# Performance work log

Hardware: AMD Instinct MI355X
Metric: run time of the kernel (lower is better)

## Reference

```python
import jax, jax.numpy as jnp
import numpy as np


def setup_inputs() -> dict:
    key = jax.random.key(0)
    k1, k2 = jax.random.split(key)
    B, P, D = 32, 512, 384
    x = jax.random.normal(k1, (B, P, D), dtype=jnp.float32)
    duration = jax.random.randint(k2, (B, P), 0, 5, dtype=jnp.int32)
    return {"x": x, "duration": duration, "max_len": 2048}


def reference(x, duration, max_len):
    # x: [B, P, D], duration: [B, P] int, max_len: python int
    B, P, D = x.shape
    dur = duration.astype(jnp.int32)
    ends = jnp.cumsum(dur, axis=1)          # [B, P] exclusive end offsets per phoneme
    mel_lens = ends[:, -1]                   # [B] total frames per utterance
    t = jnp.arange(max_len, dtype=jnp.int32)
    # frame t belongs to phoneme i where ends[i-1] <= t < ends[i]
    idx = jax.vmap(lambda e: jnp.searchsorted(e, t, side='right'))(ends)  # [B, T]
    idx = jnp.clip(idx, 0, P - 1)
    out = jnp.take_along_axis(x, idx[..., None], axis=1)  # [B, T, D]
    mask = (t[None, :] < mel_lens[:, None])[..., None]     # zero out padding frames
    out = jnp.where(mask, out, jnp.zeros((), dtype=x.dtype))
    return out, mel_lens
```

## Files before the change

### kernel.cpp

```cpp
#include <hip/hip_runtime.h>

#define LR_B      32
#define LR_P      512
#define LR_D      384
#define LR_MAXLEN 2048
#define LR_V4     (LR_D / 4)

__global__ __launch_bounds__(LR_P) void lr_scan_idx(
    const int* __restrict__ dur,
    int* __restrict__ idx_out,
    float* __restrict__ mel_out)
{
    const int b   = blockIdx.x;
    const int tid = threadIdx.x;

    __shared__ int s[LR_P];
    s[tid] = dur[b * LR_P + tid];
    __syncthreads();

    #pragma unroll
    for (int off = 1; off < LR_P; off <<= 1) {
        int v = (tid >= off) ? s[tid - off] : 0;
        __syncthreads();
        s[tid] += v;
        __syncthreads();
    }

    const int mel = s[LR_P - 1];
    if (tid == 0) mel_out[b] = (float)mel;

    #pragma unroll
    for (int k = 0; k < LR_MAXLEN / LR_P; ++k) {
        const int t = tid + k * LR_P;
        int r;
        if (t >= mel) {
            r = -1;
        } else {
            int lo = 0, hi = LR_P;
            while (lo < hi) {
                int mid = (lo + hi) >> 1;
                if (s[mid] <= t) lo = mid + 1; else hi = mid;
            }
            r = lo;
        }
        idx_out[b * LR_MAXLEN + t] = r;
    }
}

__global__ __launch_bounds__(256) void lr_gather(
    const float4* __restrict__ x4,
    const int*    __restrict__ idx,
    float4*       __restrict__ out4)
{
    const int gid   = blockIdx.x * 256 + threadIdx.x;
    const int frame = gid / LR_V4;
    const int v     = gid - frame * LR_V4;

    const int p = idx[frame];
    float4 val;
    if (p >= 0) {
        const int b = frame >> 11;
        val = x4[(b * LR_P + p) * LR_V4 + v];
    } else {
        val = make_float4(0.f, 0.f, 0.f, 0.f);
    }
    out4[gid] = val;
}

extern "C" void kernel_launch(void* const* d_in, const int* in_sizes, int n_in,
                              void* d_out, int out_size, void* d_ws, size_t ws_size,
                              hipStream_t stream)
{
    const float* x   = (const float*)d_in[0];
    const int*   dur = (const int*)d_in[1];

    float* out = (float*)d_out;
    float* mel = out + (size_t)LR_B * LR_MAXLEN * LR_D;

    int* ws_idx = (int*)d_ws;

    lr_scan_idx<<<LR_B, LR_P, 0, stream>>>(dur, ws_idx, mel);

    const int total4 = LR_B * LR_MAXLEN * LR_V4;
    lr_gather<<<total4 / 256, 256, 0, stream>>>(
        (const float4*)x, ws_idx, (float4*)out);
}
```

Measured before the change: 28.78 us.

## Use wave-shuffle scan, two float4s per thread, XCD remap and nontemporal stores

The block-wide shared-memory scan is replaced with a wavefront shuffle scan plus a small cross-wave prefix, which cuts the number of barriers. The gather kernel now has each thread move two float4 halves of a frame, so it launches half as many blocks. Block IDs are remapped so that each of the 8 XCDs handles a contiguous chunk. Outputs are written with nontemporal stores to avoid polluting the cache. These changes target memory-bound write bandwidth and scan latency, and they reduce the number of threads available to hide memory latency.

```diff
diff --git a/kernel.cpp b/kernel.cpp
--- a/kernel.cpp
+++ b/kernel.cpp
@@ -5,28 +5,42 @@
 #define LR_D      384
 #define LR_MAXLEN 2048
 #define LR_V4     (LR_D / 4)
+#define LR_HV4    (LR_V4 / 2)
+
+typedef float f32x4 __attribute__((ext_vector_type(4)));
 
 __global__ __launch_bounds__(LR_P) void lr_scan_idx(
     const int* __restrict__ dur,
     int* __restrict__ idx_out,
     float* __restrict__ mel_out)
 {
-    const int b   = blockIdx.x;
-    const int tid = threadIdx.x;
+    const int b    = blockIdx.x;
+    const int tid  = threadIdx.x;
+    const int lane = tid & 63;
+    const int wid  = tid >> 6;
 
-    __shared__ int s[LR_P];
-    s[tid] = dur[b * LR_P + tid];
+    __shared__ int ends[LR_P];
+    __shared__ int wsum[LR_P / 64];
+
+    int v = dur[b * LR_P + tid];
+
+    #pragma unroll
+    for (int off = 1; off < 64; off <<= 1) {
+        int u = __shfl_up(v, off, 64);
+        if (lane >= off) v += u;
+    }
+    if (lane == 63) wsum[wid] = v;
     __syncthreads();
 
+    int woff = 0;
     #pragma unroll
-    for (int off = 1; off < LR_P; off <<= 1) {
-        int v = (tid >= off) ? s[tid - off] : 0;
-        __syncthreads();
-        s[tid] += v;
-        __syncthreads();
-    }
+    for (int i = 0; i < LR_P / 64; ++i)
+        woff += (i < wid) ? wsum[i] : 0;
+    v += woff;
+    ends[tid] = v;
+    __syncthreads();
 
-    const int mel = s[LR_P - 1];
+    const int mel = ends[LR_P - 1];
     if (tid == 0) mel_out[b] = (float)mel;
 
     #pragma unroll
@@ -39,7 +53,7 @@
             int lo = 0, hi = LR_P;
             while (lo < hi) {
                 int mid = (lo + hi) >> 1;
-                if (s[mid] <= t) lo = mid + 1; else hi = mid;
+                if (ends[mid] <= t) lo = mid + 1; else hi = mid;
             }
             r = lo;
         }
@@ -47,24 +61,36 @@
     }
 }
 
+#define LR_GBLOCKS ((LR_B * LR_MAXLEN * LR_HV4) / 256)
+#define LR_NXCD    8
+#define LR_CHUNK   (LR_GBLOCKS / LR_NXCD)
+
 __global__ __launch_bounds__(256) void lr_gather(
-    const float4* __restrict__ x4,
-    const int*    __restrict__ idx,
-    float4*       __restrict__ out4)
+    const f32x4* __restrict__ x4,
+    const int*   __restrict__ idx,
+    f32x4*       __restrict__ out4)
 {
-    const int gid   = blockIdx.x * 256 + threadIdx.x;
-    const int frame = gid / LR_V4;
-    const int v     = gid - frame * LR_V4;
+    const int bid = blockIdx.x;
+    const int lb  = (bid & (LR_NXCD - 1)) * LR_CHUNK + (bid >> 3);
+
+    const int gid   = lb * 256 + threadIdx.x;
+    const int frame = gid / LR_HV4;
+    const int v0    = gid - frame * LR_HV4;
 
     const int p = idx[frame];
-    float4 val;
+    f32x4 a, c;
     if (p >= 0) {
-        const int b = frame >> 11;
-        val = x4[(b * LR_P + p) * LR_V4 + v];
+        const int b    = frame >> 11;
+        const int base = (b * LR_P + p) * LR_V4 + v0;
+        a = x4[base];
+        c = x4[base + LR_HV4];
     } else {
-        val = make_float4(0.f, 0.f, 0.f, 0.f);
+        a = (f32x4){0.f, 0.f, 0.f, 0.f};
+        c = a;
     }
-    out4[gid] = val;
+    const int obase = frame * LR_V4 + v0;
+    __builtin_nontemporal_store(a, &out4[obase]);
+    __builtin_nontemporal_store(c, &out4[obase + LR_HV4]);
 }
 
 extern "C" void kernel_launch(void* const* d_in, const int* in_sizes, int n_in,
@@ -81,7 +107,6 @@
 
     lr_scan_idx<<<LR_B, LR_P, 0, stream>>>(dur, ws_idx, mel);
 
-    const int total4 = LR_B * LR_MAXLEN * LR_V4;
-    lr_gather<<<total4 / 256, 256, 0, stream>>>(
-        (const float4*)x, ws_idx, (float4*)out);
+    lr_gather<<<LR_GBLOCKS, 256, 0, stream>>>(
+        (const f32x4*)x, ws_idx, (f32x4*)out);
 }
```

Result: faster. 26.74 us (-7.1%).

## Fuse duration scan and frame gather into one kernel with per-block recomputed scan

Applied to the files above, without the earlier changes.

Replaces the two-kernel pipeline (block scan plus binary search writing an index buffer, then a gather) with a single kernel. Each block recomputes the wavefront-shuffle prefix sum over its utterance's durations and scatters phoneme indices for its 32-frame chunk into shared memory, so the workspace round trip and one launch disappear. Blocks are remapped across XCDs so that chunks of the same utterance land on the same XCD, and output stores use nontemporal hints. In exchange, the duration scan is recomputed redundantly in every block.

```diff
diff --git a/kernel.cpp b/kernel.cpp
--- a/kernel.cpp
+++ b/kernel.cpp
@@ -5,66 +5,88 @@
 #define LR_D      384
 #define LR_MAXLEN 2048
 #define LR_V4     (LR_D / 4)
+#define LR_FPB    32
+#define LR_F4PB   (LR_FPB * LR_V4)
+#define LR_THREADS 256
+#define LR_F4PT   (LR_F4PB / LR_THREADS)
 
-__global__ __launch_bounds__(LR_P) void lr_scan_idx(
-    const int* __restrict__ dur,
-    int* __restrict__ idx_out,
-    float* __restrict__ mel_out)
+#define LR_CHUNKS  (LR_MAXLEN / LR_FPB)
+#define LR_GBLOCKS (LR_B * LR_CHUNKS)
+#define LR_NXCD    8
+#define LR_CPX     (LR_GBLOCKS / LR_NXCD)
+
+typedef float f32x4 __attribute__((ext_vector_type(4)));
+
+__global__ __launch_bounds__(LR_THREADS) void lr_fused(
+    const int*   __restrict__ dur,
+    const f32x4* __restrict__ x4,
+    f32x4*       __restrict__ out4,
+    float*       __restrict__ mel_out)
 {
-    const int b   = blockIdx.x;
-    const int tid = threadIdx.x;
+    const int bid = blockIdx.x;
+    const int lb  = (bid & (LR_NXCD - 1)) * LR_CPX + (bid >> 3);
 
-    __shared__ int s[LR_P];
-    s[tid] = dur[b * LR_P + tid];
+    const int b    = lb >> 6;
+    const int c    = lb & 63;
+    const int base = c * LR_FPB;
+
+    const int tid  = threadIdx.x;
+    const int lane = tid & 63;
+    const int wid  = tid >> 6;
+
+    __shared__ int smem_idx[LR_FPB];
+    __shared__ int wsum[LR_THREADS / 64];
+
+    if (tid < LR_FPB) smem_idx[tid] = -1;
+
+    const int2 d2 = ((const int2*)(dur + b * LR_P))[tid];
+    const int  e0 = d2.x, e1 = d2.y;
+    int s = e0 + e1;
+
+    #pragma unroll
+    for (int off = 1; off < 64; off <<= 1) {
+        int u = __shfl_up(s, off, 64);
+        if (lane >= off) s += u;
+    }
+    if (lane == 63) wsum[wid] = s;
     __syncthreads();
 
+    int woff = 0, total = 0;
     #pragma unroll
-    for (int off = 1; off < LR_P; off <<= 1) {
-        int v = (tid >= off) ? s[tid - off] : 0;
-        __syncthreads();
-        s[tid] += v;
-        __syncthreads();
+    for (int i = 0; i < LR_THREADS / 64; ++i) {
+        int w = wsum[i];
+        woff  += (i < wid) ? w : 0;
+        total += w;
     }
+    const int ends1  = s + woff;
+    const int ends0  = ends1 - e1;
+    const int start0 = ends0 - e0;
 
-    const int mel = s[LR_P - 1];
-    if (tid == 0) mel_out[b] = (float)mel;
+    {
+        int lo = max(start0, base), hi = min(ends0, base + LR_FPB);
+        for (int f = lo; f < hi; ++f) smem_idx[f - base] = 2 * tid;
+        lo = max(ends0, base);  hi = min(ends1, base + LR_FPB);
+        for (int f = lo; f < hi; ++f) smem_idx[f - base] = 2 * tid + 1;
+    }
+    if (c == 0 && tid == 0) mel_out[b] = (float)total;
+    __syncthreads();
 
+    const f32x4* xb    = x4 + (size_t)b * LR_P * LR_V4;
+    f32x4*       ob    = out4 + ((size_t)b * LR_MAXLEN + base) * LR_V4;
     #pragma unroll
-    for (int k = 0; k < LR_MAXLEN / LR_P; ++k) {
-        const int t = tid + k * LR_P;
-        int r;
-        if (t >= mel) {
-            r = -1;
+    for (int k = 0; k < LR_F4PT; ++k) {
+        const unsigned j     = tid + k * LR_THREADS;
+        const unsigned frame = j / LR_V4;
+        const unsigned v     = j - frame * LR_V4;
+        const int p = smem_idx[frame];
+        f32x4 val;
+        if (p >= 0) {
+            val = xb[(unsigned)p * LR_V4 + v];
         } else {
-            int lo = 0, hi = LR_P;
-            while (lo < hi) {
-                int mid = (lo + hi) >> 1;
-                if (s[mid] <= t) lo = mid + 1; else hi = mid;
-            }
-            r = lo;
+            val = (f32x4){0.f, 0.f, 0.f, 0.f};
         }
-        idx_out[b * LR_MAXLEN + t] = r;
+        __builtin_nontemporal_store(val, &ob[j]);
     }
-}
-
-__global__ __launch_bounds__(256) void lr_gather(
-    const float4* __restrict__ x4,
-    const int*    __restrict__ idx,
-    float4*       __restrict__ out4)
-{
-    const int gid   = blockIdx.x * 256 + threadIdx.x;
-    const int frame = gid / LR_V4;
-    const int v     = gid - frame * LR_V4;
-
-    const int p = idx[frame];
-    float4 val;
-    if (p >= 0) {
-        const int b = frame >> 11;
-        val = x4[(b * LR_P + p) * LR_V4 + v];
-    } else {
-        val = make_float4(0.f, 0.f, 0.f, 0.f);
-    }
-    out4[gid] = val;
 }
 
 extern "C" void kernel_launch(void* const* d_in, const int* in_sizes, int n_in,
@@ -77,11 +99,6 @@
     float* out = (float*)d_out;
     float* mel = out + (size_t)LR_B * LR_MAXLEN * LR_D;
 
-    int* ws_idx = (int*)d_ws;
-
-    lr_scan_idx<<<LR_B, LR_P, 0, stream>>>(dur, ws_idx, mel);
-
-    const int total4 = LR_B * LR_MAXLEN * LR_V4;
-    lr_gather<<<total4 / 256, 256, 0, stream>>>(
-        (const float4*)x, ws_idx, (float4*)out);
+    lr_fused<<<LR_GBLOCKS, LR_THREADS, 0, stream>>>(
+        dur, (const f32x4*)x, (f32x4*)out, mel);
 }
```

After: 25.23 us. 12.3% less time.
